# Kernel optimization log

Measured on AMD Instinct MI355X. Metric: run time of the kernel, lower is better.

Reference implementation:

```python
import jax, jax.numpy as jnp
import numpy as np

NUM_USERS = 100000
NUM_ITEMS = 50000
N = NUM_USERS + NUM_ITEMS
EMB = 64
NNZ = 4000000
B = 4096
GAMMA = 1.0
REG_LAMBDA = 1e-4
T_END = 1.0  # Euler step size: t = [0, 1]
EPS = 1e-12


def setup_inputs() -> dict:
    key = jax.random.key(0)
    ks = jax.random.split(key, 8)
    user = jax.random.randint(ks[0], (B,), 0, NUM_USERS)
    positive = jax.random.randint(ks[1], (B,), 0, NUM_ITEMS)
    negative = jax.random.randint(ks[2], (B,), 0, NUM_ITEMS)
    adj_rows = jax.random.randint(ks[3], (NNZ,), 0, N)
    adj_cols = jax.random.randint(ks[4], (NNZ,), 0, N)
    # normalized-adjacency-like small positive values
    adj_vals = jax.random.uniform(ks[5], (NNZ,), jnp.float32) * 1e-3
    user_emb = jax.random.normal(ks[6], (NUM_USERS, EMB), jnp.float32) * 0.1
    item_emb = jax.random.normal(ks[7], (NUM_ITEMS, EMB), jnp.float32) * 0.1
    return {
        "user": user, "positive": positive, "negative": negative,
        "adj_rows": adj_rows, "adj_cols": adj_cols, "adj_vals": adj_vals,
        "user_emb": user_emb, "item_emb": item_emb,
    }


def _normalize(x):
    return x * jax.lax.rsqrt(jnp.sum(x * x, axis=-1, keepdims=True) + EPS)


def _uniform_loss(x):
    # log mean_{i<j} exp(-2 * ||xn_i - xn_j||^2), xn = L2-normalized
    xn = _normalize(x)
    sq = jnp.maximum(2.0 - 2.0 * (xn @ xn.T), 0.0)  # [B, B] pairwise squared dist
    mask = jnp.triu(jnp.ones((x.shape[0], x.shape[0]), bool), k=1)
    vals = jnp.where(mask, jnp.exp(-2.0 * sq), 0.0)
    n_pairs = x.shape[0] * (x.shape[0] - 1) / 2.0
    return jnp.log(jnp.sum(vals) / n_pairs)


def reference(user, positive, negative, adj_rows, adj_cols, adj_vals, user_emb, item_emb):
    # ego embeddings: concat user/item tables -> [N, EMB]
    x = jnp.concatenate([user_emb, item_emb], axis=0)
    # sparse spmm: ax = A @ x (COO gather + segment reduce)
    ax = jax.ops.segment_sum(adj_vals[:, None] * x[adj_cols], adj_rows, num_segments=N)
    # ODEFunc f(t, x) = A@x + e with e = x0; one Euler step z1 = x0 + t*(A@x0 + x0)
    z = x + T_END * (ax + x)
    u_all, i_all = z[:NUM_USERS], z[NUM_USERS:]
    u = u_all[user]          # [B, EMB]
    i = i_all[positive]      # [B, EMB]
    # alignment loss on normalized embeddings
    un, inn = _normalize(u), _normalize(i)
    align = jnp.mean(jnp.sum((un - inn) ** 2, axis=-1))
    # uniformity loss
    uniform = GAMMA * (_uniform_loss(u) + _uniform_loss(i)) / 2.0
    # L2 reg on ego (pre-propagation) embeddings
    ego_u = user_emb[user]
    ego_i = item_emb[positive]
    reg = REG_LAMBDA * 0.5 * (jnp.sum(ego_u ** 2) + jnp.sum(ego_i ** 2)) / B
    return jnp.stack([align, uniform, reg])
```

## Files before the change

### kernel.cpp

```cpp
#include <hip/hip_runtime.h>
#include <math.h>

#define NUSERS 100000
#define NITEMS 50000
#define NN (NUSERS + NITEMS)
#define EMB 64
#define NNZ_ 4000000
#define BB 4096
#define NSLOT (2 * BB)
#define CAP 128
#define FSTR 32
#define BMW 4688
#define EPSN 1e-12f
#define NT 32
#define NTRI 528
#define NG (NNZ_ / 4)
#define SGRID 2048


typedef __attribute__((ext_vector_type(8))) short short8v;
typedef __attribute__((ext_vector_type(16))) float f32x16;

__device__ inline float wave_reduce_sum(float v) {
  #pragma unroll
  for (int off = 32; off >= 1; off >>= 1) v += __shfl_xor(v, off, 64);
  return v;
}

__device__ inline unsigned short f2bf(float f) {
  unsigned u = __float_as_uint(f);
  unsigned r = u + 0x7fffu + ((u >> 16) & 1u);
  return (unsigned short)(r >> 16);
}

__global__ __launch_bounds__(256) void lg_init(int* map, int* fillp, unsigned* bitmap) {
  int t = blockIdx.x * blockDim.x + threadIdx.x;
  if (t < NN) map[t] = -1;
  if (t < NSLOT * FSTR) fillp[t] = 0;
  if (t < BMW) bitmap[t] = 0u;
}

__global__ __launch_bounds__(256) void lg_mark(const int* __restrict__ user,
                                               const int* __restrict__ positive,
                                               int* __restrict__ map,
                                               unsigned* __restrict__ bitmap) {
  int t = blockIdx.x * blockDim.x + threadIdx.x;
  if (t >= 2 * BB) return;
  int row = (t < BB) ? user[t] : (NUSERS + positive[t - BB]);
  atomicCAS(&map[row], -1, t);
  atomicOr(&bitmap[row >> 5], 1u << (row & 31));
}

__global__ __launch_bounds__(256) void lg_scan_bin(const int4* __restrict__ rows4,
                                                   const int* __restrict__ cols,
                                                   const float* __restrict__ vals,
                                                   const unsigned* __restrict__ bitmap,
                                                   const int* __restrict__ map,
                                                   int* __restrict__ fillp,
                                                   uint2* __restrict__ bins) {
  __shared__ int qr[4][512];
  __shared__ int qk[4][512];
  int t = threadIdx.x;
  int lane = t & 63, w = t >> 6;
  unsigned long long lmlt = (1ull << lane) - 1ull;
  const int STR = SGRID * 256;
  int g0 = blockIdx.x * 256 + t;
  int g1 = g0 + STR;
  bool v1 = g1 < NG;
  int4 r0 = rows4[g0];
  int4 r1 = v1 ? rows4[g1] : make_int4(0, 0, 0, 0);
  bool h0 = ((bitmap[r0.x >> 5] >> (r0.x & 31)) & 1u);
  bool h1 = ((bitmap[r0.y >> 5] >> (r0.y & 31)) & 1u);
  bool h2 = ((bitmap[r0.z >> 5] >> (r0.z & 31)) & 1u);
  bool h3 = ((bitmap[r0.w >> 5] >> (r0.w & 31)) & 1u);
  bool h4 = v1 && ((bitmap[r1.x >> 5] >> (r1.x & 31)) & 1u);
  bool h5 = v1 && ((bitmap[r1.y >> 5] >> (r1.y & 31)) & 1u);
  bool h6 = v1 && ((bitmap[r1.z >> 5] >> (r1.z & 31)) & 1u);
  bool h7 = v1 && ((bitmap[r1.w >> 5] >> (r1.w & 31)) & 1u);
  int k0 = g0 * 4, k1 = g1 * 4;
  int qn = 0;
  #define ENQ(hh, rr, kk)                                                   \
  {                                                                         \
    unsigned long long m = __ballot(hh);                                    \
    if (hh) { int p = qn + (int)__popcll(m & lmlt); qr[w][p] = (rr);        \
              qk[w][p] = (kk); }                                            \
    qn += (int)__popcll(m);                                                 \
  }
  ENQ(h0, r0.x, k0 + 0)
  ENQ(h1, r0.y, k0 + 1)
  ENQ(h2, r0.z, k0 + 2)
  ENQ(h3, r0.w, k0 + 3)
  ENQ(h4, r1.x, k1 + 0)
  ENQ(h5, r1.y, k1 + 1)
  ENQ(h6, r1.z, k1 + 2)
  ENQ(h7, r1.w, k1 + 3)
  #undef ENQ
  for (int i = lane; i < qn; i += 64) {
    int rr = qr[w][i];
    int kk = qk[w][i];
    int s = map[rr];
    int c = cols[kk];
    float fv = vals[kk];
    int pos = atomicAdd(&fillp[s * FSTR], 1);
    if (pos < CAP) bins[(size_t)s * CAP + pos] = make_uint2((unsigned)c, __float_as_uint(fv));
  }
}

__global__ __launch_bounds__(256) void lg_accum(const int* __restrict__ fillp,
                                                const uint2* __restrict__ bins,
                                                const float* __restrict__ uemb,
                                                const float* __restrict__ iemb,
                                                float* __restrict__ acc) {
  int w = (blockIdx.x * blockDim.x + threadIdx.x) >> 6;
  int lane = threadIdx.x & 63;
  if (w >= NSLOT) return;
  int n = min(fillp[w * FSTR], CAP);
  const uint2* bs = bins + (size_t)w * CAP;
  float a = 0.0f;
  int k = 0;
  for (; k + 4 <= n; k += 4) {
    uint2 e0 = bs[k];
    uint2 e1 = bs[k + 1];
    uint2 e2 = bs[k + 2];
    uint2 e3 = bs[k + 3];
    int c0 = (int)e0.x; float v0 = __uint_as_float(e0.y);
    int c1 = (int)e1.x; float v1 = __uint_as_float(e1.y);
    int c2 = (int)e2.x; float v2 = __uint_as_float(e2.y);
    int c3 = (int)e3.x; float v3 = __uint_as_float(e3.y);
    const float* x0 = (c0 < NUSERS) ? uemb + (size_t)c0 * EMB : iemb + (size_t)(c0 - NUSERS) * EMB;
    const float* x1 = (c1 < NUSERS) ? uemb + (size_t)c1 * EMB : iemb + (size_t)(c1 - NUSERS) * EMB;
    const float* x2 = (c2 < NUSERS) ? uemb + (size_t)c2 * EMB : iemb + (size_t)(c2 - NUSERS) * EMB;
    const float* x3 = (c3 < NUSERS) ? uemb + (size_t)c3 * EMB : iemb + (size_t)(c3 - NUSERS) * EMB;
    float f0 = x0[lane], f1 = x1[lane], f2 = x2[lane], f3 = x3[lane];
    a = fmaf(v0, f0, a);
    a = fmaf(v1, f1, a);
    a = fmaf(v2, f2, a);
    a = fmaf(v3, f3, a);
  }
  for (; k < n; ++k) {
    uint2 e0 = bs[k];
    int c0 = (int)e0.x; float v0 = __uint_as_float(e0.y);
    const float* x0 = (c0 < NUSERS) ? uemb + (size_t)c0 * EMB : iemb + (size_t)(c0 - NUSERS) * EMB;
    a = fmaf(v0, x0[lane], a);
  }
  acc[(size_t)w * EMB + lane] = a;
}

__global__ __launch_bounds__(256) void lg_prep(const int* __restrict__ user,
                                               const int* __restrict__ positive,
                                               const float* __restrict__ uemb,
                                               const float* __restrict__ iemb,
                                               const int* __restrict__ map,
                                               const float* __restrict__ acc,
                                               unsigned short* __restrict__ zub,
                                               unsigned short* __restrict__ zib,
                                               float* __restrict__ part_align,
                                               float* __restrict__ part_reg) {
  int w = (blockIdx.x * blockDim.x + threadIdx.x) >> 6;
  int lane = threadIdx.x & 63;
  if (w >= BB) return;
  int ru = user[w];
  int pi = positive[w];
  float eu = uemb[(size_t)ru * EMB + lane];
  float ei = iemb[(size_t)pi * EMB + lane];
  int su = map[ru];
  int si = map[NUSERS + pi];
  float zul = 2.0f * eu + acc[(size_t)su * EMB + lane];
  float zil = 2.0f * ei + acc[(size_t)si * EMB + lane];
  float nu = wave_reduce_sum(zul * zul);
  float ni = wave_reduce_sum(zil * zil);
  float un = zul * rsqrtf(nu + EPSN);
  float inn = zil * rsqrtf(ni + EPSN);
  zub[(size_t)w * EMB + lane] = f2bf(un);
  zib[(size_t)w * EMB + lane] = f2bf(inn);
  float d = un - inn;
  float align_b = wave_reduce_sum(d * d);
  float reg_b = wave_reduce_sum(eu * eu + ei * ei);
  if (lane == 0) {
    part_align[w] = align_b;
    part_reg[w] = reg_b;
  }
}

__global__ __launch_bounds__(256) void lg_gram_mfma(const unsigned short* __restrict__ zub,
                                                    const unsigned short* __restrict__ zib,
                                                    float* __restrict__ gpart) {
  int L = blockIdx.x, m = blockIdx.y;
  int ib = 0, rem = L;
  while (rem >= NT - ib) { rem -= NT - ib; ++ib; }
  int jb = ib + rem;
  const unsigned short* z = (m == 0) ? zub : zib;
  __shared__ uint4 As4[1024];
  __shared__ uint4 Bs4[1024];
  __shared__ float wsum[4];
  int t = threadIdx.x;
  const uint4* srcA = (const uint4*)(z + (size_t)ib * 128 * EMB);
  const uint4* srcB = (const uint4*)(z + (size_t)jb * 128 * EMB);
  #pragma unroll
  for (int it = 0; it < 4; ++it) {
    int idx = it * 256 + t;
    int r = idx >> 3, s = idx & 7;
    int dst = r * 8 + (s ^ (r & 7));
    As4[dst] = srcA[idx];
    Bs4[dst] = srcB[idx];
  }
  __syncthreads();
  int l = t & 63, w = t >> 6;
  int wr = w >> 1, wc = w & 1;
  int lr = l & 31;
  int h = l >> 5;
  int ra0 = wr * 64 + lr;
  int ra1 = ra0 + 32;
  int rb0 = wc * 64 + lr;
  int rb1 = rb0 + 32;
  f32x16 a00 = {}, a01 = {}, a10 = {}, a11 = {};
  #pragma unroll
  for (int ks = 0; ks < 4; ++ks) {
    int seg = ks * 2 + h;
    short8v a0 = *(const short8v*)&As4[ra0 * 8 + (seg ^ (ra0 & 7))];
    short8v a1 = *(const short8v*)&As4[ra1 * 8 + (seg ^ (ra1 & 7))];
    short8v b0 = *(const short8v*)&Bs4[rb0 * 8 + (seg ^ (rb0 & 7))];
    short8v b1 = *(const short8v*)&Bs4[rb1 * 8 + (seg ^ (rb1 & 7))];
    a00 = __builtin_amdgcn_mfma_f32_32x32x16_bf16(a0, b0, a00, 0, 0, 0);
    a01 = __builtin_amdgcn_mfma_f32_32x32x16_bf16(a0, b1, a01, 0, 0, 0);
    a10 = __builtin_amdgcn_mfma_f32_32x32x16_bf16(a1, b0, a10, 0, 0, 0);
    a11 = __builtin_amdgcn_mfma_f32_32x32x16_bf16(a1, b1, a11, 0, 0, 0);
  }
  float s = 0.0f;
  #pragma unroll
  for (int e = 0; e < 16; ++e) {
    s += __expf(-2.0f * fmaxf(fmaf(-2.0f, a00[e], 2.0f), 0.0f));
    s += __expf(-2.0f * fmaxf(fmaf(-2.0f, a01[e], 2.0f), 0.0f));
    s += __expf(-2.0f * fmaxf(fmaf(-2.0f, a10[e], 2.0f), 0.0f));
    s += __expf(-2.0f * fmaxf(fmaf(-2.0f, a11[e], 2.0f), 0.0f));
  }
  s = wave_reduce_sum(s);
  if (l == 0) wsum[w] = s;
  __syncthreads();
  if (t == 0) {
    float tot = wsum[0] + wsum[1] + wsum[2] + wsum[3];
    float wgt = (ib == jb) ? 1.0f : 2.0f;
    gpart[m * NTRI + L] = wgt * tot;
  }
}

__global__ __launch_bounds__(256) void lg_final(const float* __restrict__ part_align,
                                                const float* __restrict__ part_reg,
                                                const float* __restrict__ gpart,
                                                float* __restrict__ out) {
  __shared__ float red[4][4];
  int t = threadIdx.x;
  float sa = 0.0f, sr = 0.0f, su = 0.0f, si = 0.0f;
  for (int k = t; k < 4096; k += 256) {
    sa += part_align[k];
    sr += part_reg[k];
  }
  for (int k = t; k < NTRI; k += 256) {
    su += gpart[k];
    si += gpart[NTRI + k];
  }
  sa = wave_reduce_sum(sa);
  sr = wave_reduce_sum(sr);
  su = wave_reduce_sum(su);
  si = wave_reduce_sum(si);
  if ((t & 63) == 0) {
    int wid = t >> 6;
    red[wid][0] = sa; red[wid][1] = sr; red[wid][2] = su; red[wid][3] = si;
  }
  __syncthreads();
  if (t == 0) {
    float a = 0, r = 0, Su = 0, Si = 0;
    #pragma unroll
    for (int wv = 0; wv < 4; ++wv) {
      a += red[wv][0]; r += red[wv][1]; Su += red[wv][2]; Si += red[wv][3];
    }
    float align = a / (float)BB;
    float reg = 1e-4f * 0.5f * r / (float)BB;
    float npairs = (float)BB * (float)(BB - 1) * 0.5f;
    float tri_u = (Su - (float)BB) * 0.5f;
    float tri_i = (Si - (float)BB) * 0.5f;
    float Lu = logf(tri_u / npairs);
    float Li = logf(tri_i / npairs);
    out[0] = align;
    out[1] = 0.5f * (Lu + Li);
    out[2] = reg;
  }
}

extern "C" void kernel_launch(void* const* d_in, const int* in_sizes, int n_in,
                              void* d_out, int out_size, void* d_ws, size_t ws_size,
                              hipStream_t stream) {
  const int* user = (const int*)d_in[0];
  const int* positive = (const int*)d_in[1];
  const int* adj_rows = (const int*)d_in[3];
  const int* adj_cols = (const int*)d_in[4];
  const float* adj_vals = (const float*)d_in[5];
  const float* uemb = (const float*)d_in[6];
  const float* iemb = (const float*)d_in[7];

  char* ws = (char*)d_ws;
  int* map = (int*)(ws);
  int* fillp = (int*)(ws + (1u << 20));
  uint2* bins = (uint2*)(ws + (2u << 20));
  float* acc = (float*)(ws + (10u << 20));
  unsigned short* zub = (unsigned short*)(ws + (12u << 20));
  unsigned short* zib = (unsigned short*)(ws + (12u << 20) + (512u << 10));
  float* part_align = (float*)(ws + (13u << 20));
  float* part_reg = (float*)(ws + (13u << 20) + (16u << 10));
  float* gpart = (float*)(ws + (13u << 20) + (32u << 10));
  unsigned* bitmap = (unsigned*)(ws + (13u << 20) + (64u << 10));
  float* out = (float*)d_out;

  lg_init<<<dim3(1024), dim3(256), 0, stream>>>(map, fillp, bitmap);
  lg_mark<<<dim3(32), dim3(256), 0, stream>>>(user, positive, map, bitmap);
  lg_scan_bin<<<dim3(SGRID), dim3(256), 0, stream>>>(
      (const int4*)adj_rows, adj_cols, adj_vals, bitmap, map, fillp, bins);
  lg_accum<<<dim3(NSLOT / 4), dim3(256), 0, stream>>>(fillp, bins, uemb, iemb, acc);
  lg_prep<<<dim3(1024), dim3(256), 0, stream>>>(user, positive, uemb, iemb, map,
                                                acc, zub, zib, part_align, part_reg);
  lg_gram_mfma<<<dim3(NTRI, 2), dim3(256), 0, stream>>>(zub, zib, gpart);
  lg_final<<<dim3(1), dim3(256), 0, stream>>>(part_align, part_reg, gpart, out);
}
```

Before: 60.86 us.

## Fuse final reduction into gram kernel, shrink init, drop padded fill counters

Folds the single-block final reduction into the gram kernel through a last-block-done atomic counter, which removes one kernel launch. The init kernel no longer writes -1 into the 150K-entry map, and the mark kernel uses plain stores instead of atomicCAS. The fill counters lose their 32-int padding, so the init work drops to 52 blocks. In exchange, duplicate rows now resolve to whichever slot's store lands last rather than deterministically, and the unpadded counters may see more atomic contention on shared cache lines.

```diff
diff --git a/kernel.cpp b/kernel.cpp
--- a/kernel.cpp
+++ b/kernel.cpp
@@ -9,7 +9,6 @@
 #define BB 4096
 #define NSLOT (2 * BB)
 #define CAP 128
-#define FSTR 32
 #define BMW 4688
 #define EPSN 1e-12f
 #define NT 32
@@ -33,11 +32,11 @@
   return (unsigned short)(r >> 16);
 }
 
-__global__ __launch_bounds__(256) void lg_init(int* map, int* fillp, unsigned* bitmap) {
+__global__ __launch_bounds__(256) void lg_init(int* fillp, unsigned* bitmap, int* done) {
   int t = blockIdx.x * blockDim.x + threadIdx.x;
-  if (t < NN) map[t] = -1;
-  if (t < NSLOT * FSTR) fillp[t] = 0;
+  if (t < NSLOT) fillp[t] = 0;
   if (t < BMW) bitmap[t] = 0u;
+  if (t == 0) *done = 0;
 }
 
 __global__ __launch_bounds__(256) void lg_mark(const int* __restrict__ user,
@@ -47,7 +46,7 @@
   int t = blockIdx.x * blockDim.x + threadIdx.x;
   if (t >= 2 * BB) return;
   int row = (t < BB) ? user[t] : (NUSERS + positive[t - BB]);
-  atomicCAS(&map[row], -1, t);
+  map[row] = t;
   atomicOr(&bitmap[row >> 5], 1u << (row & 31));
 }
 
@@ -101,7 +100,7 @@
     int s = map[rr];
     int c = cols[kk];
     float fv = vals[kk];
-    int pos = atomicAdd(&fillp[s * FSTR], 1);
+    int pos = atomicAdd(&fillp[s], 1);
     if (pos < CAP) bins[(size_t)s * CAP + pos] = make_uint2((unsigned)c, __float_as_uint(fv));
   }
 }
@@ -114,7 +113,7 @@
   int w = (blockIdx.x * blockDim.x + threadIdx.x) >> 6;
   int lane = threadIdx.x & 63;
   if (w >= NSLOT) return;
-  int n = min(fillp[w * FSTR], CAP);
+  int n = min(fillp[w], CAP);
   const uint2* bs = bins + (size_t)w * CAP;
   float a = 0.0f;
   int k = 0;
@@ -184,7 +183,11 @@
 
 __global__ __launch_bounds__(256) void lg_gram_mfma(const unsigned short* __restrict__ zub,
                                                     const unsigned short* __restrict__ zib,
-                                                    float* __restrict__ gpart) {
+                                                    float* __restrict__ gpart,
+                                                    int* __restrict__ done,
+                                                    const float* __restrict__ part_align,
+                                                    const float* __restrict__ part_reg,
+                                                    float* __restrict__ out) {
   int L = blockIdx.x, m = blockIdx.y;
   int ib = 0, rem = L;
   while (rem >= NT - ib) { rem -= NT - ib; ++ib; }
@@ -193,6 +196,7 @@
   __shared__ uint4 As4[1024];
   __shared__ uint4 Bs4[1024];
   __shared__ float wsum[4];
+  __shared__ int lastflag;
   int t = threadIdx.x;
   const uint4* srcA = (const uint4*)(z + (size_t)ib * 128 * EMB);
   const uint4* srcB = (const uint4*)(z + (size_t)jb * 128 * EMB);
@@ -241,15 +245,14 @@
     float tot = wsum[0] + wsum[1] + wsum[2] + wsum[3];
     float wgt = (ib == jb) ? 1.0f : 2.0f;
     gpart[m * NTRI + L] = wgt * tot;
-  }
-}
-
-__global__ __launch_bounds__(256) void lg_final(const float* __restrict__ part_align,
-                                                const float* __restrict__ part_reg,
-                                                const float* __restrict__ gpart,
-                                                float* __restrict__ out) {
+    __threadfence();
+    int old = atomicAdd(done, 1);
+    lastflag = (old == 2 * NTRI - 1);
+  }
+  __syncthreads();
+  if (!lastflag) return;
+  __threadfence();
   __shared__ float red[4][4];
-  int t = threadIdx.x;
   float sa = 0.0f, sr = 0.0f, su = 0.0f, si = 0.0f;
   for (int k = t; k < 4096; k += 256) {
     sa += part_align[k];
@@ -263,9 +266,8 @@
   sr = wave_reduce_sum(sr);
   su = wave_reduce_sum(su);
   si = wave_reduce_sum(si);
-  if ((t & 63) == 0) {
-    int wid = t >> 6;
-    red[wid][0] = sa; red[wid][1] = sr; red[wid][2] = su; red[wid][3] = si;
+  if (l == 0) {
+    red[w][0] = sa; red[w][1] = sr; red[w][2] = su; red[w][3] = si;
   }
   __syncthreads();
   if (t == 0) {
@@ -308,16 +310,17 @@
   float* part_align = (float*)(ws + (13u << 20));
   float* part_reg = (float*)(ws + (13u << 20) + (16u << 10));
   float* gpart = (float*)(ws + (13u << 20) + (32u << 10));
+  int* done = (int*)(ws + (13u << 20) + (56u << 10));
   unsigned* bitmap = (unsigned*)(ws + (13u << 20) + (64u << 10));
   float* out = (float*)d_out;
 
-  lg_init<<<dim3(1024), dim3(256), 0, stream>>>(map, fillp, bitmap);
+  lg_init<<<dim3(52), dim3(256), 0, stream>>>(fillp, bitmap, done);
   lg_mark<<<dim3(32), dim3(256), 0, stream>>>(user, positive, map, bitmap);
   lg_scan_bin<<<dim3(SGRID), dim3(256), 0, stream>>>(
       (const int4*)adj_rows, adj_cols, adj_vals, bitmap, map, fillp, bins);
   lg_accum<<<dim3(NSLOT / 4), dim3(256), 0, stream>>>(fillp, bins, uemb, iemb, acc);
   lg_prep<<<dim3(1024), dim3(256), 0, stream>>>(user, positive, uemb, iemb, map,
                                                 acc, zub, zib, part_align, part_reg);
-  lg_gram_mfma<<<dim3(NTRI, 2), dim3(256), 0, stream>>>(zub, zib, gpart);
-  lg_final<<<dim3(1), dim3(256), 0, stream>>>(part_align, part_reg, gpart, out);
-}
+  lg_gram_mfma<<<dim3(NTRI, 2), dim3(256), 0, stream>>>(zub, zib, gpart, done,
+                                                        part_align, part_reg, out);
+}
```

Result: slower. 76.78 us (+26.2%).
